# Kernel optimization log

Measured on AMD Instinct MI355X. Metric: run time of the kernel, lower is better.

The kernel has to match this reference:

```python
import jax, jax.numpy as jnp
import numpy as np

FEATURE_DIM = 1024
HIDDEN_DIM = FEATURE_DIM // 4  # MetaNet default: max(input_dim//4, output_dim) = 256
NUM_TASKS = 8
BATCH = 8192


def setup_inputs() -> dict:
    key = jax.random.key(0)
    ks = jax.random.split(key, 8)
    features = jax.random.normal(ks[0], (BATCH, FEATURE_DIM), dtype=jnp.float32)
    # meta_net: Linear(D->H) -> ReLU -> Linear(H->K). Scaled so coefficients straddle the threshold.
    W1 = jax.random.normal(ks[1], (HIDDEN_DIM, FEATURE_DIM), dtype=jnp.float32) * 0.02
    b1 = jax.random.normal(ks[2], (HIDDEN_DIM,), dtype=jnp.float32) * 0.01
    W2 = jax.random.normal(ks[3], (NUM_TASKS, HIDDEN_DIM), dtype=jnp.float32) * 0.1
    b2 = jax.random.normal(ks[4], (NUM_TASKS,), dtype=jnp.float32) * 0.05
    # per-task feature transforms, init randn * 0.01 as in the module
    task_mats = jax.random.normal(ks[5], (NUM_TASKS, FEATURE_DIM, FEATURE_DIM), dtype=jnp.float32) * 0.01
    # projection initialized to identity (nn.init.eye_)
    proj_W = jnp.eye(FEATURE_DIM, dtype=jnp.float32)
    base_threshold = jnp.array([0.05], dtype=jnp.float32)
    beta = jnp.array([1.0], dtype=jnp.float32)
    return {"features": features, "W1": W1, "b1": b1, "W2": W2, "b2": b2,
            "task_mats": task_mats, "proj_W": proj_W,
            "base_threshold": base_threshold, "beta": beta}


def reference(features, W1, b1, W2, b2, task_mats, proj_W, base_threshold, beta):
    # --- meta_net forward: coefficients [B, K] ---
    h = features @ W1.T + b1                    # [B, H]
    relu_h = jnp.maximum(h, 0.0)
    coeffs = relu_h @ W2.T + b2                 # [B, K]

    # --- gradient-based uncertainty: ||d coeff_k / d features_b||_2 ---
    # Jacobian of the 2-layer MLP: J[b,k,d] = sum_h W2[k,h] * relu'(h[b,h]) * W1[h,d]
    mask = (h > 0).astype(features.dtype)       # [B, H]
    J = jnp.einsum('kh,bh,hd->bkd', W2, mask, W1)   # [B, K, D]
    unc = jnp.sqrt(jnp.sum(J * J, axis=-1))     # [B, K]
    mx = jnp.max(unc)
    unc = jnp.where(mx > 0, unc / mx, unc)
    # torch computes this on detached features with create_graph=False -> non-differentiable
    unc = jax.lax.stop_gradient(unc)

    # --- adaptive gating ---
    base = jax.nn.softplus(base_threshold)                  # [1]
    thresholds = base * (1.0 + jax.nn.relu(beta) * unc)     # [B, K]
    gated = jnp.where(jnp.abs(coeffs) < thresholds, 0.0, coeffs)  # [B, K]

    # --- sequential weighted task-vector combination (blockwise=False) ---
    x = features                                # [B, D]
    for j in range(task_mats.shape[0]):         # small fixed K, structurally sequential
        x = x + gated[:, j:j + 1] * (x @ task_mats[j])
    return x @ proj_W.T                         # [B, D]
```

## Files before the change

kernel.cpp:

```cpp
#include <hip/hip_runtime.h>


typedef float  f32x4  __attribute__((ext_vector_type(4)));
typedef __bf16 bf16x8 __attribute__((ext_vector_type(8)));
typedef _Float16 f16x8 __attribute__((ext_vector_type(8)));
typedef _Float16 f16x4 __attribute__((ext_vector_type(4)));

__device__ __forceinline__ unsigned short f2bf(float x) {
  return __builtin_bit_cast(unsigned short, (__bf16)x);
}
__device__ __forceinline__ float bf2f(unsigned short u) {
  return (float)__builtin_bit_cast(__bf16, u);
}
__device__ __forceinline__ void ldsload16(void* lds, const void* g) {
  __builtin_amdgcn_global_load_lds(
      (const __attribute__((address_space(1))) void*)g,
      (__attribute__((address_space(3))) void*)lds, 16, 0, 0);
}


__global__ __launch_bounds__(256) void k_initsplit(const float* __restrict__ F,
                                                   _Float16* __restrict__ hi,
                                                   _Float16* __restrict__ lo,
                                                   float* __restrict__ xout,
                                                   unsigned short* __restrict__ xh) {
  size_t i = (size_t)blockIdx.x * 256 + threadIdx.x;
  float4 f = *(const float4*)&F[i * 4];
  _Float16 h0 = (_Float16)f.x, h1 = (_Float16)f.y, h2 = (_Float16)f.z, h3 = (_Float16)f.w;
  *(f16x4*)&hi[i * 4] = (f16x4){h0, h1, h2, h3};
  *(f16x4*)&lo[i * 4] = (f16x4){(_Float16)((f.x - (float)h0) * 2048.0f),
                                (_Float16)((f.y - (float)h1) * 2048.0f),
                                (_Float16)((f.z - (float)h2) * 2048.0f),
                                (_Float16)((f.w - (float)h3) * 2048.0f)};
  *(float4*)&xout[i * 4] = f;
  ushort4 u;
  u.x = f2bf(f.x); u.y = f2bf(f.y); u.z = f2bf(f.z); u.w = f2bf(f.w);
  *(ushort4*)&xh[i * 4] = u;
}

__global__ __launch_bounds__(256) void k_split(const float* __restrict__ src,
                                               _Float16* __restrict__ hi,
                                               _Float16* __restrict__ lo) {
  size_t i = (size_t)blockIdx.x * 256 + threadIdx.x;
  float4 f = *(const float4*)&src[i * 4];
  _Float16 h0 = (_Float16)f.x, h1 = (_Float16)f.y, h2 = (_Float16)f.z, h3 = (_Float16)f.w;
  *(f16x4*)&hi[i * 4] = (f16x4){h0, h1, h2, h3};
  *(f16x4*)&lo[i * 4] = (f16x4){(_Float16)((f.x - (float)h0) * 2048.0f),
                                (_Float16)((f.y - (float)h1) * 2048.0f),
                                (_Float16)((f.z - (float)h2) * 2048.0f),
                                (_Float16)((f.w - (float)h3) * 2048.0f)};
}

__global__ __launch_bounds__(256) void k_gram(const float* __restrict__ W1,
                                              float* __restrict__ G) {
  __shared__ float Wa[16][33], Wb[16][33];
  int t = threadIdx.x, ti = t & 15, tj = t >> 4;
  int bi = blockIdx.x, bj = blockIdx.y;
  float acc = 0.f;
  for (int kc = 0; kc < 1024; kc += 32) {
    __syncthreads();
    for (int e = t; e < 512; e += 256) {
      int r = e >> 5, k = e & 31;
      Wa[r][k] = W1[(size_t)(bi * 16 + r) * 1024 + kc + k];
      Wb[r][k] = W1[(size_t)(bj * 16 + r) * 1024 + kc + k];
    }
    __syncthreads();
#pragma unroll
    for (int k = 0; k < 32; k++) acc += Wa[ti][k] * Wb[tj][k];
  }
  G[(size_t)(bi * 16 + ti) * 256 + bj * 16 + tj] = acc;
}

__global__ __launch_bounds__(256) void k_prepA(const float* __restrict__ W2,
                                               const float* __restrict__ G,
                                               unsigned short* __restrict__ Bk) {
  int k = blockIdx.x >> 8, hr = blockIdx.x & 255, t = threadIdx.x;
  float v = W2[k * 256 + hr] * W2[k * 256 + t] * G[(size_t)hr * 256 + t];
  float hi = bf2f(f2bf(v));
  float lo = v - hi;
  unsigned short* row = &Bk[((size_t)k * 256 + hr) * 512];
  row[t] = f2bf(hi);
  row[256 + t] = f2bf(lo);
}

__global__ __launch_bounds__(256) void k_maskcoef(const float* __restrict__ h,
                                                  const float* __restrict__ W2,
                                                  const float* __restrict__ b2,
                                                  unsigned short* __restrict__ Mb,
                                                  unsigned int* __restrict__ Mbits,
                                                  float* __restrict__ coeffs) {
  __shared__ float W2s[2048];
  __shared__ unsigned sw[4][8];
  int t = threadIdx.x;
  for (int e = t; e < 2048; e += 256) W2s[e] = W2[e];
  int w = t >> 6, l = t & 63;
  int row = blockIdx.x * 4 + w;
  float4 hv = *(const float4*)&h[(size_t)row * 256 + l * 4];
  ushort4 mv;
  mv.x = hv.x > 0.f ? 0x3F80 : 0; mv.y = hv.y > 0.f ? 0x3F80 : 0;
  mv.z = hv.z > 0.f ? 0x3F80 : 0; mv.w = hv.w > 0.f ? 0x3F80 : 0;
  *(ushort4*)&Mb[(size_t)row * 256 + l * 4] = mv;
  unsigned nib = (hv.x > 0.f ? 1u : 0u) | (hv.y > 0.f ? 2u : 0u) |
                 (hv.z > 0.f ? 4u : 0u) | (hv.w > 0.f ? 8u : 0u);
  if (l < 8) sw[w][l] = 0u;
  __syncthreads();
  atomicOr(&sw[w][l >> 3], nib << ((l & 7) * 4));
  __syncthreads();
  if (l < 8) Mbits[row * 8 + l] = sw[w][l];
  float r0 = fmaxf(hv.x, 0.f), r1 = fmaxf(hv.y, 0.f);
  float r2 = fmaxf(hv.z, 0.f), r3 = fmaxf(hv.w, 0.f);
#pragma unroll
  for (int k = 0; k < 8; k++) {
    const float* wr = &W2s[k * 256 + l * 4];
    float p = r0 * wr[0] + r1 * wr[1] + r2 * wr[2] + r3 * wr[3];
    p += __shfl_xor(p, 1);  p += __shfl_xor(p, 2);  p += __shfl_xor(p, 4);
    p += __shfl_xor(p, 8);  p += __shfl_xor(p, 16); p += __shfl_xor(p, 32);
    if (l == 0) coeffs[row * 8 + k] = p + b2[k];
  }
}

__global__ __launch_bounds__(256) void k_max(const float* __restrict__ unc2,
                                             unsigned int* __restrict__ mx) {
  int i = blockIdx.x * 256 + threadIdx.x;
  float v = 0.f;
  for (; i < 65536; i += 64 * 256) v = fmaxf(v, unc2[i]);
#pragma unroll
  for (int d = 1; d < 64; d <<= 1) v = fmaxf(v, __shfl_xor(v, d));
  __shared__ float sm[4];
  if ((threadIdx.x & 63) == 0) sm[threadIdx.x >> 6] = v;
  __syncthreads();
  if (threadIdx.x == 0) {
    v = fmaxf(fmaxf(sm[0], sm[1]), fmaxf(sm[2], sm[3]));
    atomicMax(mx, __float_as_uint(v));
  }
}

__global__ __launch_bounds__(256) void k_gateidx(const float* __restrict__ coeffs,
                                                 const float* __restrict__ unc2,
                                                 const unsigned int* __restrict__ mxb,
                                                 const float* __restrict__ btp,
                                                 const float* __restrict__ betap,
                                                 float* __restrict__ gated,
                                                 unsigned short* __restrict__ rowidx,
                                                 int* __restrict__ cnt) {
  __shared__ int lc[8], base[8];
  int t = threadIdx.x;
  if (t < 8) lc[t] = 0;
  __syncthreads();
  int i = blockIdx.x * 256 + t;
  float c = coeffs[i];
  float u2 = fmaxf(unc2[i], 0.f);
  float un = sqrtf(u2);
  float m = sqrtf(__uint_as_float(*mxb));
  float u = (m > 0.f) ? un / m : un;
  float base_t = (float)log1p(exp((double)btp[0]));
  float br = fmaxf(betap[0], 0.f);
  float thr = base_t * (1.0f + br * u);
  float gv = (fabsf(c) < thr) ? 0.f : c;
  gated[i] = gv;
  int jj = i & 7, row = i >> 3, slot = -1;
  if (gv != 0.f) slot = atomicAdd(&lc[jj], 1);
  __syncthreads();
  if (t < 8) base[t] = lc[t] ? atomicAdd(&cnt[t], lc[t]) : 0;
  __syncthreads();
  if (slot >= 0) rowidx[jj * 8192 + base[jj] + slot] = (unsigned short)row;
}

__global__ __launch_bounds__(256) void k_prepT(const float* __restrict__ TM,
                                               unsigned short* __restrict__ Tb) {
  __shared__ float Ls[64][65];
  int bid = blockIdx.x;
  int jj = bid >> 8, kt = (bid >> 4) & 15, nt = bid & 15;
  int t = threadIdx.x;
  int r = t >> 2, c0 = (t & 3) * 16;
  const float* src = TM + (size_t)jj * 1048576 + (size_t)(kt * 64 + r) * 1024 + nt * 64 + c0;
  float4 v0 = *(const float4*)&src[0];
  float4 v1 = *(const float4*)&src[4];
  float4 v2 = *(const float4*)&src[8];
  float4 v3 = *(const float4*)&src[12];
  float tmp[16] = {v0.x, v0.y, v0.z, v0.w, v1.x, v1.y, v1.z, v1.w,
                   v2.x, v2.y, v2.z, v2.w, v3.x, v3.y, v3.z, v3.w};
#pragma unroll
  for (int i = 0; i < 16; i++) Ls[r][c0 + i] = tmp[i];
  __syncthreads();
  int nr = t >> 2, kc = (t & 3) * 16;
  union { unsigned short s[16]; uint4 v[2]; } p;
#pragma unroll
  for (int i = 0; i < 16; i++) p.s[i] = f2bf(Ls[kc + i][nr]);
  unsigned short* dst = Tb + (size_t)jj * 1048576 + (size_t)(nt * 64 + nr) * 1024 + kt * 64 + kc;
  *(uint4*)&dst[0] = p.v[0];
  *(uint4*)&dst[8] = p.v[1];
}

__global__ __launch_bounds__(256) void k_prepP(const float* __restrict__ P,
                                               unsigned short* __restrict__ Pb) {
  size_t i = (size_t)blockIdx.x * 256 + threadIdx.x;
  float4 f = *(const float4*)&P[i * 4];
  ushort4 u;
  u.x = f2bf(f.x); u.y = f2bf(f.y); u.z = f2bf(f.z); u.w = f2bf(f.w);
  *(ushort4*)&Pb[i * 4] = u;
}

__global__ __launch_bounds__(256) void k_checkP(const float* __restrict__ P,
                                                unsigned int* __restrict__ flag) {
  size_t i = (size_t)blockIdx.x * 256 + threadIdx.x;
  float4 v = *(const float4*)&P[i * 4];
  size_t e = i * 4;
  bool bad = false;
#pragma unroll
  for (int s = 0; s < 4; s++) {
    size_t ee = e + s;
    float exp = ((ee >> 10) == (ee & 1023)) ? 1.0f : 0.0f;
    float got = (s == 0) ? v.x : (s == 1) ? v.y : (s == 2) ? v.z : v.w;
    if (got != exp) bad = true;
  }
  if (bad) atomicAnd(flag, 0u);
}


__global__ __launch_bounds__(256) void k_gemm_h2(const _Float16* __restrict__ Fhi,
                                                 const _Float16* __restrict__ Flo,
                                                 const _Float16* __restrict__ W1h,
                                                 const _Float16* __restrict__ W1l,
                                                 const float* __restrict__ b1,
                                                 float* __restrict__ hout) {
  __shared__ __attribute__((aligned(16))) _Float16 Ah[64 * 32];
  __shared__ __attribute__((aligned(16))) _Float16 Al[64 * 32];
  __shared__ __attribute__((aligned(16))) _Float16 Bh[64 * 32];
  __shared__ __attribute__((aligned(16))) _Float16 Bl[64 * 32];
  int t = threadIdx.x, w = t >> 6, l = t & 63, q = l >> 4, li = l & 15;
  int wm = w >> 1, wn = w & 1;
  int ib = blockIdx.x, jb = blockIdx.y;
  f32x4 acc0[2][2] = {}, acc1[2][2] = {};
  int row = t >> 2, kc = (t & 3) * 8;
  for (int k0 = 0; k0 < 1024; k0 += 32) {
    __syncthreads();
    size_t ao = (size_t)(ib * 64 + row) * 1024 + k0 + kc;
    size_t bo = (size_t)(jb * 64 + row) * 1024 + k0 + kc;
    ldsload16((void*)(Ah + (w * 64) * 8), Fhi + ao);
    ldsload16((void*)(Al + (w * 64) * 8), Flo + ao);
    ldsload16((void*)(Bh + (w * 64) * 8), W1h + bo);
    ldsload16((void*)(Bl + (w * 64) * 8), W1l + bo);
    __syncthreads();
    f16x8 ah[2], al[2], bh[2], bl[2];
#pragma unroll
    for (int mt = 0; mt < 2; mt++) {
      ah[mt] = *(const f16x8*)&Ah[(wm * 32 + mt * 16 + li) * 32 + q * 8];
      al[mt] = *(const f16x8*)&Al[(wm * 32 + mt * 16 + li) * 32 + q * 8];
    }
#pragma unroll
    for (int nt = 0; nt < 2; nt++) {
      bh[nt] = *(const f16x8*)&Bh[(wn * 32 + nt * 16 + li) * 32 + q * 8];
      bl[nt] = *(const f16x8*)&Bl[(wn * 32 + nt * 16 + li) * 32 + q * 8];
    }
#pragma unroll
    for (int mt = 0; mt < 2; mt++)
#pragma unroll
      for (int nt = 0; nt < 2; nt++) {
        acc0[mt][nt] = __builtin_amdgcn_mfma_f32_16x16x32_f16(ah[mt], bh[nt], acc0[mt][nt], 0, 0, 0);
        acc1[mt][nt] = __builtin_amdgcn_mfma_f32_16x16x32_f16(ah[mt], bl[nt], acc1[mt][nt], 0, 0, 0);
        acc1[mt][nt] = __builtin_amdgcn_mfma_f32_16x16x32_f16(al[mt], bh[nt], acc1[mt][nt], 0, 0, 0);
      }
  }
  const float sc = 1.0f / 2048.0f;
#pragma unroll
  for (int mt = 0; mt < 2; mt++) {
    int grow = ib * 64 + wm * 32 + mt * 16 + q * 4;
#pragma unroll
    for (int nt = 0; nt < 2; nt++) {
      int gcol = jb * 64 + wn * 32 + nt * 16 + li;
      float bb = b1[gcol];
#pragma unroll
      for (int r = 0; r < 4; r++)
        hout[(size_t)(grow + r) * 256 + gcol] = acc0[mt][nt][r] + acc1[mt][nt][r] * sc + bb;
    }
  }
}

__global__ __launch_bounds__(256) void k_gemm_unc(const unsigned short* __restrict__ Mb,
                                                  const unsigned short* __restrict__ BkAll,
                                                  const unsigned int* __restrict__ Mbits,
                                                  float* __restrict__ unc2) {
  __shared__ __attribute__((aligned(16))) unsigned short As[64 * 32];
  __shared__ __attribute__((aligned(16))) unsigned short Bs[256 * 32];
  int t = threadIdx.x, w = t >> 6, l = t & 63, q = l >> 4, li = l & 15;
  int rb = blockIdx.x, kidx = blockIdx.y;
  const unsigned short* Bk = BkAll + (size_t)kidx * 256 * 512;
  f32x4 acc[16] = {};
  for (int k0 = 0; k0 < 512; k0 += 32) {
    __syncthreads();
    {
      int row = t >> 2, kc = (t & 3) * 8;
      int kk = (k0 & 255) + kc;
      ldsload16((void*)(As + (w * 64) * 8), Mb + (size_t)(rb * 64 + row) * 256 + kk);
    }
#pragma unroll
    for (int i = 0; i < 4; i++) {
      int idx = i * 256 + t, row = idx >> 2, kc = (idx & 3) * 8;
      ldsload16((void*)(Bs + (i * 256 + w * 64) * 8), Bk + (size_t)row * 512 + k0 + kc);
    }
    __syncthreads();
    bf16x8 av = *(const bf16x8*)&As[(w * 16 + li) * 32 + q * 8];
#pragma unroll
    for (int nt = 0; nt < 16; nt++) {
      bf16x8 bv = *(const bf16x8*)&Bs[(nt * 16 + li) * 32 + q * 8];
      acc[nt] = __builtin_amdgcn_mfma_f32_16x16x32_bf16(av, bv, acc[nt], 0, 0, 0);
    }
  }
  int row0 = rb * 64 + w * 16 + q * 4;
  unsigned mw[4][8];
#pragma unroll
  for (int r = 0; r < 4; r++) {
    const uint4* p = (const uint4*)&Mbits[(size_t)(row0 + r) * 8];
    uint4 a = p[0], b = p[1];
    mw[r][0] = a.x; mw[r][1] = a.y; mw[r][2] = a.z; mw[r][3] = a.w;
    mw[r][4] = b.x; mw[r][5] = b.y; mw[r][6] = b.z; mw[r][7] = b.w;
  }
  float ps[4] = {0.f, 0.f, 0.f, 0.f};
#pragma unroll
  for (int nt = 0; nt < 16; nt++) {
    int word = nt >> 1, sh = (nt & 1) * 16 + li;
#pragma unroll
    for (int r = 0; r < 4; r++)
      if ((mw[r][word] >> sh) & 1u) ps[r] += acc[nt][r];
  }
#pragma unroll
  for (int r = 0; r < 4; r++) {
    float v = ps[r];
    v += __shfl_xor(v, 1); v += __shfl_xor(v, 2);
    v += __shfl_xor(v, 4); v += __shfl_xor(v, 8);
    ps[r] = v;
  }
  if (li == 0)
#pragma unroll
    for (int r = 0; r < 4; r++) unc2[(size_t)(row0 + r) * 8 + kidx] = ps[r];
}

__global__ __launch_bounds__(256) void k_chain_sp2(const unsigned short* __restrict__ xh,
                                                   float* __restrict__ Cp,
                                                   const unsigned short* __restrict__ Tb,
                                                   const unsigned short* __restrict__ rowidx,
                                                   const int* __restrict__ cnt, int j) {
  int Mj = cnt[j];
  int ib = blockIdx.x;
  if (ib * 128 >= Mj) return;
  __shared__ __attribute__((aligned(16))) unsigned short As[128 * 32];
  __shared__ __attribute__((aligned(16))) unsigned short Bs[128 * 32];
  int t = threadIdx.x, w = t >> 6, l = t & 63, q = l >> 4, li = l & 15;
  int wm = w >> 1, wn = w & 1;
  int jb = blockIdx.y, kz = blockIdx.z;
  int lr = t >> 2, kcol = (t & 3) * 8;
  int cm0 = ib * 128 + lr, cm1 = cm0 + 64;
  int g0 = rowidx[j * 8192 + (cm0 < Mj ? cm0 : Mj - 1)];
  int g1 = rowidx[j * 8192 + (cm1 < Mj ? cm1 : Mj - 1)];
  const unsigned short* a0 = xh + (size_t)g0 * 1024 + kz * 256 + kcol;
  const unsigned short* a1 = xh + (size_t)g1 * 1024 + kz * 256 + kcol;
  f32x4 acc[4][4] = {};
  for (int k0 = 0; k0 < 256; k0 += 32) {
    uint4 va = *(const uint4*)(a0 + k0);
    uint4 vb = *(const uint4*)(a1 + k0);
    const unsigned short* gb = Tb + (size_t)(jb * 128) * 1024 + kz * 256 + k0;
    __syncthreads();
#pragma unroll
    for (int i = 0; i < 2; i++) {
      int idx = i * 256 + t, row = idx >> 2, kc = (idx & 3) * 8;
      ldsload16((void*)(Bs + (i * 256 + w * 64) * 8), gb + (size_t)row * 1024 + kc);
    }
    *(uint4*)&As[lr * 32 + kcol] = va;
    *(uint4*)&As[(lr + 64) * 32 + kcol] = vb;
    __syncthreads();
    bf16x8 av[4], bv[4];
#pragma unroll
    for (int mt = 0; mt < 4; mt++)
      av[mt] = *(const bf16x8*)&As[(wm * 64 + mt * 16 + li) * 32 + q * 8];
#pragma unroll
    for (int nt = 0; nt < 4; nt++)
      bv[nt] = *(const bf16x8*)&Bs[(wn * 64 + nt * 16 + li) * 32 + q * 8];
#pragma unroll
    for (int mt = 0; mt < 4; mt++)
#pragma unroll
      for (int nt = 0; nt < 4; nt++)
        acc[mt][nt] = __builtin_amdgcn_mfma_f32_16x16x32_bf16(av[mt], bv[nt], acc[mt][nt], 0, 0, 0);
  }
  float* cpz = Cp + (size_t)kz * 8192 * 1024;
#pragma unroll
  for (int mt = 0; mt < 4; mt++) {
    int crow = ib * 128 + wm * 64 + mt * 16 + q * 4;
#pragma unroll
    for (int nt = 0; nt < 4; nt++) {
      int gcol = jb * 128 + wn * 64 + nt * 16 + li;
#pragma unroll
      for (int r = 0; r < 4; r++) {
        int cm = crow + r;
        if (cm < Mj) cpz[(size_t)cm * 1024 + gcol] = acc[mt][nt][r];
      }
    }
  }
}

__global__ __launch_bounds__(256) void k_chain_upd2(const float* __restrict__ Cp,
                                                    const unsigned short* __restrict__ rowidx,
                                                    const int* __restrict__ cnt,
                                                    const float* __restrict__ gated,
                                                    float* __restrict__ xout,
                                                    unsigned short* __restrict__ xh, int j) {
  int Mj = cnt[j];
  int t = threadIdx.x;
  int c0 = t * 4;
  const size_t plane = (size_t)8192 * 1024;
  for (int cm = blockIdx.x; cm < Mj; cm += gridDim.x) {
    int row = rowidx[j * 8192 + cm];
    float g = gated[row * 8 + j];
    size_t co = (size_t)cm * 1024 + c0;
    float4 s0 = *(const float4*)&Cp[co];
    float4 s1 = *(const float4*)&Cp[co + plane];
    float4 s2 = *(const float4*)&Cp[co + 2 * plane];
    float4 s3 = *(const float4*)&Cp[co + 3 * plane];
    float4 xv = *(float4*)&xout[(size_t)row * 1024 + c0];
    xv.x = fmaf(g, (s0.x + s1.x) + (s2.x + s3.x), xv.x);
    xv.y = fmaf(g, (s0.y + s1.y) + (s2.y + s3.y), xv.y);
    xv.z = fmaf(g, (s0.z + s1.z) + (s2.z + s3.z), xv.z);
    xv.w = fmaf(g, (s0.w + s1.w) + (s2.w + s3.w), xv.w);
    *(float4*)&xout[(size_t)row * 1024 + c0] = xv;
    ushort4 hv;
    hv.x = f2bf(xv.x); hv.y = f2bf(xv.y); hv.z = f2bf(xv.z); hv.w = f2bf(xv.w);
    *(ushort4*)&xh[(size_t)row * 1024 + c0] = hv;
  }
}

__global__ __launch_bounds__(256) void k_proj3(const unsigned short* __restrict__ xcur,
                                               const unsigned short* __restrict__ Pb,
                                               float* __restrict__ out,
                                               const unsigned int* __restrict__ flag) {
  if (*flag) return;
  __shared__ __attribute__((aligned(16))) unsigned short As[128 * 32];
  __shared__ __attribute__((aligned(16))) unsigned short Bs[128 * 32];
  int t = threadIdx.x, w = t >> 6, l = t & 63, q = l >> 4, li = l & 15;
  int wm = w >> 1, wn = w & 1;
  int ib = blockIdx.x, jb = blockIdx.y;
  f32x4 acc[4][4] = {};
  for (int k0 = 0; k0 < 1024; k0 += 32) {
    __syncthreads();
    const unsigned short* ga = xcur + (size_t)(ib * 128) * 1024 + k0;
    const unsigned short* gb = Pb + (size_t)(jb * 128) * 1024 + k0;
#pragma unroll
    for (int i = 0; i < 2; i++) {
      int idx = i * 256 + t, row = idx >> 2, kc = (idx & 3) * 8;
      ldsload16((void*)(As + (i * 256 + w * 64) * 8), ga + (size_t)row * 1024 + kc);
      ldsload16((void*)(Bs + (i * 256 + w * 64) * 8), gb + (size_t)row * 1024 + kc);
    }
    __syncthreads();
    bf16x8 av[4], bv[4];
#pragma unroll
    for (int mt = 0; mt < 4; mt++)
      av[mt] = *(const bf16x8*)&As[(wm * 64 + mt * 16 + li) * 32 + q * 8];
#pragma unroll
    for (int nt = 0; nt < 4; nt++)
      bv[nt] = *(const bf16x8*)&Bs[(wn * 64 + nt * 16 + li) * 32 + q * 8];
#pragma unroll
    for (int mt = 0; mt < 4; mt++)
#pragma unroll
      for (int nt = 0; nt < 4; nt++)
        acc[mt][nt] = __builtin_amdgcn_mfma_f32_16x16x32_bf16(av[mt], bv[nt], acc[mt][nt], 0, 0, 0);
  }
#pragma unroll
  for (int mt = 0; mt < 4; mt++) {
    int grow = ib * 128 + wm * 64 + mt * 16 + q * 4;
#pragma unroll
    for (int nt = 0; nt < 4; nt++) {
      int gcol = jb * 128 + wn * 64 + nt * 16 + li;
#pragma unroll
      for (int r = 0; r < 4; r++)
        out[(size_t)(grow + r) * 1024 + gcol] = acc[mt][nt][r];
    }
  }
}


extern "C" void kernel_launch(void* const* d_in, const int* in_sizes, int n_in,
                              void* d_out, int out_size, void* d_ws, size_t ws_size,
                              hipStream_t stream) {
  const float* F    = (const float*)d_in[0];
  const float* W1   = (const float*)d_in[1];
  const float* b1   = (const float*)d_in[2];
  const float* W2   = (const float*)d_in[3];
  const float* b2   = (const float*)d_in[4];
  const float* TM   = (const float*)d_in[5];
  const float* PW   = (const float*)d_in[6];
  const float* bt   = (const float*)d_in[7];
  const float* beta = (const float*)d_in[8];

  char* w = (char*)d_ws;
  float*          hbuf   = (float*)         (w + 0);
  unsigned short* Mb     = (unsigned short*)(w + 8388608);
  unsigned int*   Mbits  = (unsigned int*)  (w + 12582912);
  float*          coeffs = (float*)         (w + 12845056);
  float*          unc2   = (float*)         (w + 13107200);
  float*          G      = (float*)         (w + 13369344);
  unsigned short* Bk     = (unsigned short*)(w + 13631488);
  _Float16*       W1h    = (_Float16*)      (w + 15728640);
  _Float16*       W1l    = (_Float16*)      (w + 16252928);
  unsigned short* Tb     = (unsigned short*)(w + 0);
  char*           buf0   =                  (w + 16777216);
  char*           buf1   =                  (w + 33554432);
  float*          gated  = (float*)         (w + 50331648);
  unsigned int*   mx     = (unsigned int*)  (w + 50593792);
  unsigned int*   flag   = (unsigned int*)  (w + 50593796);
  unsigned short* rowidx = (unsigned short*)(w + 50594048);
  int*            cnt    = (int*)           (w + 50725120);
  unsigned short* xh     = (unsigned short*)(w + 50855936);
  float*          Cp     = (float*)         (w + 67633152);
  float* xout = (float*)d_out;

  k_initsplit<<<8192, 256, 0, stream>>>(F, (_Float16*)buf0, (_Float16*)buf1, xout, xh);
  k_split<<<256, 256, 0, stream>>>(W1, W1h, W1l);
  k_gram<<<dim3(16, 16), 256, 0, stream>>>(W1, G);
  k_gemm_h2<<<dim3(128, 4), 256, 0, stream>>>((const _Float16*)buf0, (const _Float16*)buf1,
                                              W1h, W1l, b1, hbuf);
  k_maskcoef<<<2048, 256, 0, stream>>>(hbuf, W2, b2, Mb, Mbits, coeffs);
  k_prepA<<<2048, 256, 0, stream>>>(W2, G, Bk);
  k_gemm_unc<<<dim3(128, 8), 256, 0, stream>>>(Mb, Bk, Mbits, unc2);
  hipMemsetAsync(mx, 0, 4, stream);
  hipMemsetAsync(flag, 1, 4, stream);
  hipMemsetAsync(cnt, 0, 32, stream);
  k_max<<<64, 256, 0, stream>>>(unc2, mx);
  k_gateidx<<<256, 256, 0, stream>>>(coeffs, unc2, mx, bt, beta, gated, rowidx, cnt);

  k_prepT<<<2048, 256, 0, stream>>>(TM, Tb);
  for (int j = 0; j < 8; j++) {
    k_chain_sp2<<<dim3(64, 8, 4), 256, 0, stream>>>(xh, Cp, Tb + (size_t)j * 1048576,
                                                    rowidx, cnt, j);
    k_chain_upd2<<<512, 256, 0, stream>>>(Cp, rowidx, cnt, gated, xout, xh, j);
  }

  k_checkP<<<1024, 256, 0, stream>>>(PW, flag);
  unsigned short* Pb = (unsigned short*)buf1;
  k_prepP<<<1024, 256, 0, stream>>>(PW, Pb);
  k_proj3<<<dim3(64, 8), 256, 0, stream>>>(xh, Pb, xout, flag);
}
```

Baseline: 439.1 us.

## Fuse split-K chain update into GEMM via atomic adds, stage full K-slice in LDS

```diff
diff --git a/kernel.cpp b/kernel.cpp
--- a/kernel.cpp
+++ b/kernel.cpp
@@ -142,6 +142,7 @@
                                                  const float* __restrict__ betap,
                                                  float* __restrict__ gated,
                                                  unsigned short* __restrict__ rowidx,
+                                                 float* __restrict__ gcomp,
                                                  int* __restrict__ cnt) {
   __shared__ int lc[8], base[8];
   int t = threadIdx.x;
@@ -163,7 +164,11 @@
   __syncthreads();
   if (t < 8) base[t] = lc[t] ? atomicAdd(&cnt[t], lc[t]) : 0;
   __syncthreads();
-  if (slot >= 0) rowidx[jj * 8192 + base[jj] + slot] = (unsigned short)row;
+  if (slot >= 0) {
+    int pos = base[jj] + slot;
+    rowidx[jj * 8192 + pos] = (unsigned short)row;
+    gcomp[jj * 8192 + pos] = gv;
+  }
 }
 
 __global__ __launch_bounds__(256) void k_prepT(const float* __restrict__ TM,
@@ -336,92 +341,85 @@
     for (int r = 0; r < 4; r++) unc2[(size_t)(row0 + r) * 8 + kidx] = ps[r];
 }
 
-__global__ __launch_bounds__(256) void k_chain_sp2(const unsigned short* __restrict__ xh,
-                                                   float* __restrict__ Cp,
-                                                   const unsigned short* __restrict__ Tb,
-                                                   const unsigned short* __restrict__ rowidx,
-                                                   const int* __restrict__ cnt, int j) {
+__global__ __launch_bounds__(256) void k_chain3(const unsigned short* __restrict__ xh,
+                                                const unsigned short* __restrict__ Tb,
+                                                const unsigned short* __restrict__ rowidx,
+                                                const int* __restrict__ cnt,
+                                                const float* __restrict__ gcomp,
+                                                float* __restrict__ xout, int j) {
   int Mj = cnt[j];
   int ib = blockIdx.x;
   if (ib * 128 >= Mj) return;
-  __shared__ __attribute__((aligned(16))) unsigned short As[128 * 32];
-  __shared__ __attribute__((aligned(16))) unsigned short Bs[128 * 32];
+  __shared__ __attribute__((aligned(16))) unsigned short As[128 * 256];
+  __shared__ __attribute__((aligned(16))) unsigned short Bs[128 * 256];
   int t = threadIdx.x, w = t >> 6, l = t & 63, q = l >> 4, li = l & 15;
   int wm = w >> 1, wn = w & 1;
   int jb = blockIdx.y, kz = blockIdx.z;
-  int lr = t >> 2, kcol = (t & 3) * 8;
-  int cm0 = ib * 128 + lr, cm1 = cm0 + 64;
-  int g0 = rowidx[j * 8192 + (cm0 < Mj ? cm0 : Mj - 1)];
-  int g1 = rowidx[j * 8192 + (cm1 < Mj ? cm1 : Mj - 1)];
-  const unsigned short* a0 = xh + (size_t)g0 * 1024 + kz * 256 + kcol;
-  const unsigned short* a1 = xh + (size_t)g1 * 1024 + kz * 256 + kcol;
+  const unsigned short* ridx = rowidx + j * 8192;
+#pragma unroll
+  for (int i = 0; i < 16; i++) {
+    int slot = i * 256 + t;
+    int r = slot >> 5, kcs = slot & 31;
+    int kcg = kcs ^ (r & 7);
+    int cm = ib * 128 + r;
+    int grow = ridx[cm < Mj ? cm : Mj - 1];
+    ldsload16((void*)(As + (size_t)(i * 256 + w * 64) * 8),
+              xh + (size_t)grow * 1024 + kz * 256 + kcg * 8);
+  }
+#pragma unroll
+  for (int i = 0; i < 16; i++) {
+    int slot = i * 256 + t;
+    int n = slot >> 5, kcs = slot & 31;
+    int kcg = kcs ^ (n & 7);
+    ldsload16((void*)(Bs + (size_t)(i * 256 + w * 64) * 8),
+              Tb + (size_t)(jb * 128 + n) * 1024 + kz * 256 + kcg * 8);
+  }
+  __syncthreads();
   f32x4 acc[4][4] = {};
-  for (int k0 = 0; k0 < 256; k0 += 32) {
-    uint4 va = *(const uint4*)(a0 + k0);
-    uint4 vb = *(const uint4*)(a1 + k0);
-    const unsigned short* gb = Tb + (size_t)(jb * 128) * 1024 + kz * 256 + k0;
-    __syncthreads();
-#pragma unroll
-    for (int i = 0; i < 2; i++) {
-      int idx = i * 256 + t, row = idx >> 2, kc = (idx & 3) * 8;
-      ldsload16((void*)(Bs + (i * 256 + w * 64) * 8), gb + (size_t)row * 1024 + kc);
-    }
-    *(uint4*)&As[lr * 32 + kcol] = va;
-    *(uint4*)&As[(lr + 64) * 32 + kcol] = vb;
-    __syncthreads();
+#pragma unroll
+  for (int c0 = 0; c0 < 32; c0 += 4) {
     bf16x8 av[4], bv[4];
 #pragma unroll
-    for (int mt = 0; mt < 4; mt++)
-      av[mt] = *(const bf16x8*)&As[(wm * 64 + mt * 16 + li) * 32 + q * 8];
-#pragma unroll
-    for (int nt = 0; nt < 4; nt++)
-      bv[nt] = *(const bf16x8*)&Bs[(wn * 64 + nt * 16 + li) * 32 + q * 8];
+    for (int mt = 0; mt < 4; mt++) {
+      int r = wm * 64 + mt * 16 + li;
+      av[mt] = *(const bf16x8*)&As[((size_t)r * 32 + ((c0 + q) ^ (r & 7))) * 8];
+    }
+#pragma unroll
+    for (int nt = 0; nt < 4; nt++) {
+      int n = wn * 64 + nt * 16 + li;
+      bv[nt] = *(const bf16x8*)&Bs[((size_t)n * 32 + ((c0 + q) ^ (n & 7))) * 8];
+    }
 #pragma unroll
     for (int mt = 0; mt < 4; mt++)
 #pragma unroll
       for (int nt = 0; nt < 4; nt++)
         acc[mt][nt] = __builtin_amdgcn_mfma_f32_16x16x32_bf16(av[mt], bv[nt], acc[mt][nt], 0, 0, 0);
   }
-  float* cpz = Cp + (size_t)kz * 8192 * 1024;
 #pragma unroll
   for (int mt = 0; mt < 4; mt++) {
-    int crow = ib * 128 + wm * 64 + mt * 16 + q * 4;
-#pragma unroll
-    for (int nt = 0; nt < 4; nt++) {
-      int gcol = jb * 128 + wn * 64 + nt * 16 + li;
-#pragma unroll
-      for (int r = 0; r < 4; r++) {
-        int cm = crow + r;
-        if (cm < Mj) cpz[(size_t)cm * 1024 + gcol] = acc[mt][nt][r];
-      }
-    }
-  }
-}
-
-__global__ __launch_bounds__(256) void k_chain_upd2(const float* __restrict__ Cp,
-                                                    const unsigned short* __restrict__ rowidx,
-                                                    const int* __restrict__ cnt,
-                                                    const float* __restrict__ gated,
-                                                    float* __restrict__ xout,
-                                                    unsigned short* __restrict__ xh, int j) {
+#pragma unroll
+    for (int r = 0; r < 4; r++) {
+      int cm = ib * 128 + wm * 64 + mt * 16 + q * 4 + r;
+      if (cm >= Mj) continue;
+      int grow = ridx[cm];
+      float g = gcomp[j * 8192 + cm];
+      float* xrow = xout + (size_t)grow * 1024 + jb * 128 + wn * 64 + li;
+#pragma unroll
+      for (int nt = 0; nt < 4; nt++)
+        atomicAdd(xrow + nt * 16, g * acc[mt][nt][r]);
+    }
+  }
+}
+
+__global__ __launch_bounds__(256) void k_refresh(const float* __restrict__ xout,
+                                                 const unsigned short* __restrict__ rowidx,
+                                                 const int* __restrict__ cnt,
+                                                 unsigned short* __restrict__ xh, int j) {
   int Mj = cnt[j];
-  int t = threadIdx.x;
-  int c0 = t * 4;
-  const size_t plane = (size_t)8192 * 1024;
+  int c0 = threadIdx.x * 4;
   for (int cm = blockIdx.x; cm < Mj; cm += gridDim.x) {
     int row = rowidx[j * 8192 + cm];
-    float g = gated[row * 8 + j];
-    size_t co = (size_t)cm * 1024 + c0;
-    float4 s0 = *(const float4*)&Cp[co];
-    float4 s1 = *(const float4*)&Cp[co + plane];
-    float4 s2 = *(const float4*)&Cp[co + 2 * plane];
-    float4 s3 = *(const float4*)&Cp[co + 3 * plane];
-    float4 xv = *(float4*)&xout[(size_t)row * 1024 + c0];
-    xv.x = fmaf(g, (s0.x + s1.x) + (s2.x + s3.x), xv.x);
-    xv.y = fmaf(g, (s0.y + s1.y) + (s2.y + s3.y), xv.y);
-    xv.z = fmaf(g, (s0.z + s1.z) + (s2.z + s3.z), xv.z);
-    xv.w = fmaf(g, (s0.w + s1.w) + (s2.w + s3.w), xv.w);
-    *(float4*)&xout[(size_t)row * 1024 + c0] = xv;
+    float4 xv = *(const float4*)&xout[(size_t)row * 1024 + c0];
     ushort4 hv;
     hv.x = f2bf(xv.x); hv.y = f2bf(xv.y); hv.z = f2bf(xv.z); hv.w = f2bf(xv.w);
     *(ushort4*)&xh[(size_t)row * 1024 + c0] = hv;
@@ -509,7 +507,7 @@
   unsigned short* rowidx = (unsigned short*)(w + 50594048);
   int*            cnt    = (int*)           (w + 50725120);
   unsigned short* xh     = (unsigned short*)(w + 50855936);
-  float*          Cp     = (float*)         (w + 67633152);
+  float*          gcomp  = (float*)         (w + 67633152);
   float* xout = (float*)d_out;
 
   k_initsplit<<<8192, 256, 0, stream>>>(F, (_Float16*)buf0, (_Float16*)buf1, xout, xh);
@@ -524,13 +522,13 @@
   hipMemsetAsync(flag, 1, 4, stream);
   hipMemsetAsync(cnt, 0, 32, stream);
   k_max<<<64, 256, 0, stream>>>(unc2, mx);
-  k_gateidx<<<256, 256, 0, stream>>>(coeffs, unc2, mx, bt, beta, gated, rowidx, cnt);
+  k_gateidx<<<256, 256, 0, stream>>>(coeffs, unc2, mx, bt, beta, gated, rowidx, gcomp, cnt);
 
   k_prepT<<<2048, 256, 0, stream>>>(TM, Tb);
   for (int j = 0; j < 8; j++) {
-    k_chain_sp2<<<dim3(64, 8, 4), 256, 0, stream>>>(xh, Cp, Tb + (size_t)j * 1048576,
-                                                    rowidx, cnt, j);
-    k_chain_upd2<<<512, 256, 0, stream>>>(Cp, rowidx, cnt, gated, xout, xh, j);
+    k_chain3<<<dim3(64, 8, 4), 256, 0, stream>>>(xh, Tb + (size_t)j * 1048576,
+                                                 rowidx, cnt, gcomp, xout, j);
+    k_refresh<<<256, 256, 0, stream>>>(xout, rowidx, cnt, xh, j);
   }
 
   k_checkP<<<1024, 256, 0, stream>>>(PW, flag);
```

After: 648.3 us. +47.6%, slower.
